# Kernel tuning notes

Measured on AMD Instinct MI355X. Metric: run time of the kernel, lower is better.

Reference implementation:

```python
import jax, jax.numpy as jnp
import numpy as np

B, T, INPUT, HIDDEN = 512, 128, 64, 512
TS, PLEN = 32, 32  # attention window (time_step), decode length (predict_len)


def setup_inputs() -> dict:
    key = jax.random.key(0)
    ks = jax.random.split(key, 11)
    s = 1.0 / np.sqrt(HIDDEN)
    rn = lambda k, shape, sc: (jax.random.normal(k, shape, jnp.float32) * sc)
    return {
        "x": jax.random.normal(ks[0], (B, T, INPUT), jnp.float32),
        "W_ih": rn(ks[1], (4 * HIDDEN, INPUT), s),
        "W_hh": rn(ks[2], (4 * HIDDEN, HIDDEN), s),
        "b_lstm": rn(ks[3], (4 * HIDDEN,), s),   # b_ih + b_hh folded together
        "Wc_ih": rn(ks[4], (4 * HIDDEN, HIDDEN), s),
        "Wc_hh": rn(ks[5], (4 * HIDDEN, HIDDEN), s),
        "b_cell": rn(ks[6], (4 * HIDDEN,), s),
        "W1": rn(ks[7], (HIDDEN, 2 * HIDDEN), s),
        "b1": rn(ks[8], (HIDDEN,), s),
        "W2": rn(ks[9], (1, HIDDEN), s),
        "b2": rn(ks[10], (1,), s),
    }


def _gates_to_hc(g, c):
    # torch gate order: input, forget, cell(g), output
    i, f, gg, o = jnp.split(g, 4, axis=-1)
    c_new = jax.nn.sigmoid(f) * c + jax.nn.sigmoid(i) * jnp.tanh(gg)
    h_new = jax.nn.sigmoid(o) * jnp.tanh(c_new)
    return h_new, c_new


def reference(x, W_ih, W_hh, b_lstm, Wc_ih, Wc_hh, b_cell, W1, b1, W2, b2):
    Bx = x.shape[0]
    # ---- encoder LSTM (single layer, zero init state) ----
    x_proj = jnp.einsum('bti,gi->btg', x, W_ih) + b_lstm  # [B,T,4H]

    def enc_step(carry, xt):
        h, c = carry
        h, c = _gates_to_hc(xt + h @ W_hh.T, c)
        return (h, c), h

    z = jnp.zeros((Bx, HIDDEN), x.dtype)
    (h, c), Hs = jax.lax.scan(enc_step, (z, z), x_proj.transpose(1, 0, 2))
    Hs = Hs.transpose(1, 0, 2)  # [B,T,H]

    # ---- decode loop: LSTMCell fed its own hidden + local windowed attention ----
    # Atten only ever reads the last TS states before the newest one, so we keep
    # a rolling buffer instead of materializing the growing H.
    Wc = Wc_ih + Wc_hh  # cell input == hidden state, so the two projections fuse
    buf0 = Hs[:, -TS:, :]  # last TS encoder states

    def dec_step(carry, _):
        h, c, buf = carry
        h_t, c_t = _gates_to_hc(h @ Wc.T + b_cell, c)
        scores = jnp.einsum('bh,bsh->bs', h_t, buf)        # [B,TS]
        a = jax.nn.softmax(scores, axis=-1)
        ctx = jnp.einsum('bs,bsh->bh', a, buf)             # [B,H]
        out = jnp.concatenate([ctx, h_t], axis=-1)         # [B,2H]
        buf = jnp.concatenate([buf[:, 1:], h_t[:, None]], axis=1)
        return (h_t, c_t, buf), out

    _, outs = jax.lax.scan(dec_step, (h, c, buf0), None, length=PLEN)
    H_pre = outs.transpose(1, 0, 2)  # [B,PLEN,2H]

    # ---- fc head (dropout = eval/identity) ----
    y = jnp.tanh(H_pre @ W1.T + b1) @ W2.T + b2  # [B,PLEN,1]
    return y.squeeze(-1)
```

## Files before the change

### kernel.cpp

```cpp
#include <hip/hip_runtime.h>
#include <hip/hip_bf16.h>
#include <math.h>

#define Bz   512
#define Tz   128
#define INz  64
#define Hz   512
#define TSz  32
#define PLz  32
#define BH   (Bz * Hz)
#define NBLK 256
#define NTHR 512
#define PF   6

typedef unsigned short u16;
typedef unsigned long long u64;
typedef __attribute__((ext_vector_type(8)))  short short8;
typedef __attribute__((ext_vector_type(16))) float floatx16;

static __device__ __forceinline__ void split_bf(float w, u16& hi, u16& lo) {
    __hip_bfloat16 h = __float2bfloat16(w);
    hi = *reinterpret_cast<u16*>(&h);
    float r = w - __bfloat162float(h);
    __hip_bfloat16 l = __float2bfloat16(r);
    lo = *reinterpret_cast<u16*>(&l);
}

union FU  { unsigned u; float f; };
union F2U { u64 q; float f[2]; };

static __device__ __forceinline__ float b2f(u16 v) {
    FU c; c.u = ((unsigned)v) << 16; return c.f;
}
static __device__ __forceinline__ u16 f2b(float f) {
    __hip_bfloat16 h = __float2bfloat16(f);
    return *reinterpret_cast<u16*>(&h);
}

static __device__ __forceinline__ float aldf(const float* p) {
    FU c; c.u = __hip_atomic_load((const unsigned*)p, __ATOMIC_RELAXED, __HIP_MEMORY_SCOPE_AGENT);
    return c.f;
}
static __device__ __forceinline__ void ast64f(float* p, float a, float b) {
    F2U u; u.f[0] = a; u.f[1] = b;
    __hip_atomic_store((u64*)p, u.q, __ATOMIC_RELAXED, __HIP_MEMORY_SCOPE_AGENT);
}
static __device__ __forceinline__ void astf(float* p, float v) {
    FU c; c.f = v;
    __hip_atomic_store((unsigned*)p, c.u, __ATOMIC_RELAXED, __HIP_MEMORY_SCOPE_AGENT);
}
static __device__ __forceinline__ unsigned aldu(const unsigned* p) {
    return __hip_atomic_load(p, __ATOMIC_RELAXED, __HIP_MEMORY_SCOPE_AGENT);
}
static __device__ __forceinline__ void astu(unsigned* p, unsigned v) {
    __hip_atomic_store(p, v, __ATOMIC_RELAXED, __HIP_MEMORY_SCOPE_AGENT);
}
static __device__ __forceinline__ void astu16x2(u16* p, unsigned v) {
    __hip_atomic_store((unsigned*)p, v, __ATOMIC_RELAXED, __HIP_MEMORY_SCOPE_AGENT);
}

__global__ __launch_bounds__(256) void k_init(u16* __restrict__ h15_hi,
                                              u16* __restrict__ h15_lo,
                                              unsigned* __restrict__ sync) {
    const int i = blockIdx.x * 256 + threadIdx.x;
    if (i < BH) { h15_hi[i] = 0; h15_lo[i] = 0; }
    if (i < 8192) sync[i] = 0;
}

__global__ __launch_bounds__(256) void k_prep_wenc(const float* __restrict__ W_ih,
                                                   const float* __restrict__ W_hh,
                                                   u16* __restrict__ wf_hi,
                                                   u16* __restrict__ wf_lo) {
    const int idx = blockIdx.x * 256 + threadIdx.x;
    const int lane = idx & 63;
    const int g = (idx >> 6) % 36;
    const int cb = idx / (36 * 64);
    const int C = cb * 32 + (lane & 31);
    const int gate = ((C >> 4) & 3) * 512 + (C >> 6) * 16 + (C & 15);
    const int kh = lane >> 5;
    const size_t base = (size_t)idx * 8;
    #pragma unroll
    for (int e = 0; e < 8; ++e) {
        const int k = g * 16 + kh * 8 + e;
        const float w = (k < 64) ? W_ih[(size_t)gate * 64 + k]
                                 : W_hh[(size_t)gate * 512 + (k - 64)];
        u16 hi, lo; split_bf(w, hi, lo);
        wf_hi[base + e] = hi; wf_lo[base + e] = lo;
    }
}

__global__ __launch_bounds__(256) void k_prep_wc(const float* __restrict__ Wc_ih,
                                                 const float* __restrict__ Wc_hh,
                                                 u16* __restrict__ wf_hi,
                                                 u16* __restrict__ wf_lo) {
    const int idx = blockIdx.x * 256 + threadIdx.x;
    const int lane = idx & 63;
    const int cb = idx / (32 * 64);
    const int g = (idx >> 6) % 32;
    const int C = cb * 32 + (lane & 31);
    const int gate = ((C >> 4) & 3) * 512 + (C >> 6) * 16 + (C & 15);
    const int kh = lane >> 5;
    const size_t base = (size_t)idx * 8;
    #pragma unroll
    for (int e = 0; e < 8; ++e) {
        const int k = g * 16 + kh * 8 + e;
        const float w = Wc_ih[(size_t)gate * 512 + k] + Wc_hh[(size_t)gate * 512 + k];
        u16 hi, lo; split_bf(w, hi, lo);
        wf_hi[base + e] = hi; wf_lo[base + e] = lo;
    }
}

__global__ __launch_bounds__(256) void k_prep_w1(const float* __restrict__ W1,
                                                 u16* __restrict__ wf_hi,
                                                 u16* __restrict__ wf_lo) {
    const int idx = blockIdx.x * 256 + threadIdx.x;
    const int lane = idx & 63;
    const int cb = idx / (64 * 64);
    const int g = (idx >> 6) % 64;
    const int n = cb * 32 + (lane & 31);
    const int kh = lane >> 5;
    const size_t base = (size_t)idx * 8;
    #pragma unroll
    for (int e = 0; e < 8; ++e) {
        const int k = g * 16 + kh * 8 + e;
        const float w = W1[(size_t)n * 1024 + k];
        u16 hi, lo; split_bf(w, hi, lo);
        wf_hi[base + e] = hi; wf_lo[base + e] = lo;
    }
}

__global__ __launch_bounds__(256) void k_prep_x(const float* __restrict__ x,
                                                u16* __restrict__ xf_hi,
                                                u16* __restrict__ xf_lo) {
    const int idx = blockIdx.x * 256 + threadIdx.x;
    const int lane = idx & 63;
    const int g = (idx >> 6) & 3;
    const int rb = (idx >> 8) & 15;
    const int t = idx >> 12;
    const int b = rb * 32 + (lane & 31);
    const int kh = lane >> 5;
    const size_t base = (size_t)idx * 8;
    #pragma unroll
    for (int e = 0; e < 8; ++e) {
        const int i = g * 16 + kh * 8 + e;
        const float w = x[((size_t)b * Tz + t) * INz + i];
        u16 hi, lo; split_bf(w, hi, lo);
        xf_hi[base + e] = hi; xf_lo[base + e] = lo;
    }
}

static __device__ __forceinline__ void gsync(unsigned* sync, unsigned target, int bid) {
    __syncthreads();
    const int tid = threadIdx.x;
    unsigned* arr  = sync + 64;
    unsigned* grel = sync + 64 + 4096;
    if (bid == 0) {
        if (tid < 64) {
            if (tid == 0) astu(&arr[0], target);
            bool done = false;
            while (!done) {
                unsigned mn = 0xffffffffu;
                #pragma unroll
                for (int k = 0; k < 4; ++k) {
                    const unsigned v = aldu(&arr[(tid * 4 + k) * 16]);
                    mn = v < mn ? v : mn;
                }
                done = (bool)__all((int)(mn >= target));
                if (!done) __builtin_amdgcn_s_sleep(1);
            }
            if (tid < 16) astu(&grel[tid * 16], target);
        }
    } else {
        if (tid == 0) {
            astu(&arr[bid * 16], target);
            while (aldu(&grel[(bid >> 4) * 16]) < target)
                __builtin_amdgcn_s_sleep(1);
        }
    }
    if ((target & 15u) == 0u && tid == 0)
        __builtin_amdgcn_fence(__ATOMIC_ACQUIRE, "agent");
    __syncthreads();
}

template<int NG, int GX>
__device__ __forceinline__ void gates_phase(
    const u16* __restrict__ xf_hi, const u16* __restrict__ xf_lo, int t,
    const u16* __restrict__ wf_hi, const u16* __restrict__ wf_lo,
    const u16* __restrict__ hin_hi, const u16* __restrict__ hin_lo,
    const float* __restrict__ bias,
    float (&c2)[2], float* __restrict__ h_f32,
    u16* __restrict__ hout_hi, u16* __restrict__ hout_lo,
    u16* __restrict__ buf_enc, int slot,
    u16* A_hi, u16* A_lo, float* Gt, int ji, int bi, int tid)
{
    const int lane = tid & 63, wid = tid >> 6;
    const int wc = wid & 3, kh = wid >> 2;

    {
        float4 vh[4], vl[4];
        #pragma unroll
        for (int it = 0; it < 4; ++it) {
            const int sl = it * 512 + tid;
            const size_t off = ((size_t)bi * 32 + (sl >> 6)) * 512 + (size_t)(sl & 63) * 8;
            vh[it] = *(const float4*)(hin_hi + off);
            vl[it] = *(const float4*)(hin_lo + off);
        }
        #pragma unroll
        for (int it = 0; it < 4; ++it) {
            const int sl = it * 512 + tid;
            *(float4*)(A_hi + (size_t)sl * 8) = vh[it];
            *(float4*)(A_lo + (size_t)sl * 8) = vl[it];
        }
    }
    __syncthreads();

    constexpr int NGH = NG / 2;
    const int g0 = kh * NGH;
    const int cb = ji * 4 + wc;
    const u16* pbh = wf_hi + ((size_t)cb * NG) * 512 + lane * 8;
    const u16* pbl = wf_lo + ((size_t)cb * NG) * 512 + lane * 8;

    floatx16 acc0, acc1, acc2;
    #pragma unroll
    for (int i = 0; i < 16; ++i) { acc0[i] = 0.f; acc1[i] = 0.f; acc2[i] = 0.f; }

    short8 ah[PF], al[PF], bh[PF], bl[PF];

    #pragma unroll
    for (int i = 0; i < NGH + PF; ++i) {
        if (i >= PF) {
            const int s = (i - PF) % PF;
            acc0 = __builtin_amdgcn_mfma_f32_32x32x16_bf16(ah[s], bh[s], acc0, 0, 0, 0);
            acc1 = __builtin_amdgcn_mfma_f32_32x32x16_bf16(ah[s], bl[s], acc1, 0, 0, 0);
            acc2 = __builtin_amdgcn_mfma_f32_32x32x16_bf16(al[s], bh[s], acc2, 0, 0, 0);
        }
        if (i < NGH) {
            const int s = i % PF;
            const int g = g0 + i;
            if (GX > 0 && g < GX) {
                const size_t off = (((size_t)t * 16 + bi) * GX + g) * 512 + (size_t)lane * 8;
                ah[s] = *(const short8*)(xf_hi + off);
                al[s] = *(const short8*)(xf_lo + off);
            } else {
                const int gh = g - GX;
                ah[s] = *(const short8*)(A_hi + ((size_t)gh * 64 + lane) * 8);
                al[s] = *(const short8*)(A_lo + ((size_t)gh * 64 + lane) * 8);
            }
            bh[s] = *(const short8*)(pbh + (size_t)g * 512);
            bl[s] = *(const short8*)(pbl + (size_t)g * 512);
        }
    }
    #pragma unroll
    for (int i = 0; i < 16; ++i) acc0[i] += acc1[i] + acc2[i];

    __syncthreads();
    {
        const int col = wc * 32 + (lane & 31);
        const int rb4 = 4 * (lane >> 5);
        float* G = Gt + (size_t)kh * 4224;
        #pragma unroll
        for (int r = 0; r < 16; ++r)
            G[(rb4 + (r & 3) + 8 * (r >> 2)) * 132 + col] = acc0[r];
    }
    __syncthreads();

    {
        const int bl2 = tid >> 4, jq = tid & 15;
        const int b = bi * 32 + bl2;
        const int j0 = ji * 32 + jq * 2;
        float hn2[2];
        unsigned phi = 0, plo = 0;
        #pragma unroll
        for (int e = 0; e < 2; ++e) {
            const int jl = jq * 2 + e;
            const int Cl = ((jl >> 4) << 6) | (jl & 15);
            const float* gp = Gt + (size_t)bl2 * 132 + Cl;
            const float* gq = gp + 4224;
            const float gi = gp[0]  + gq[0]  + bias[j0 + e];
            const float gf = gp[16] + gq[16] + bias[512 + j0 + e];
            const float gg = gp[32] + gq[32] + bias[1024 + j0 + e];
            const float go = gp[48] + gq[48] + bias[1536 + j0 + e];
            const float si = 1.f / (1.f + __expf(-gi));
            const float sf = 1.f / (1.f + __expf(-gf));
            const float so = 1.f / (1.f + __expf(-go));
            const float cn = sf * c2[e] + si * tanhf(gg);
            const float hn = so * tanhf(cn);
            c2[e] = cn; hn2[e] = hn;
            u16 hi, lo; split_bf(hn, hi, lo);
            phi |= (unsigned)hi << (16 * e);
            plo |= (unsigned)lo << (16 * e);
        }
        const int gran = j0 >> 4;
        const int fl = ((j0 >> 3) & 1) * 32 + (b & 31);
        const size_t fo = (((size_t)bi * 32 + gran) * 64 + fl) * 8 + (j0 & 7);
        astu16x2(hout_hi + fo, phi);
        astu16x2(hout_lo + fo, plo);
        if (slot >= 0)
            astu16x2(buf_enc + ((size_t)b * TSz + slot) * Hz + j0, phi);
        if (h_f32 != nullptr)
            ast64f(h_f32 + (size_t)b * Hz + j0, hn2[0], hn2[1]);
    }
}

__device__ __forceinline__ void attn_phase(const float* __restrict__ h_f32,
                                           const u16* __restrict__ buf_enc,
                                           u16* __restrict__ buf_dec,
                                           u16* __restrict__ ctx_hi, u16* __restrict__ ctx_lo,
                                           int sd, float* lds, int bid, int tid) {
    const int grp = tid >> 8;
    const int t8 = tid & 255;
    const int b = bid * 2 + grp;
    float* sh = lds + grp * 544;
    float* sa = sh + 512;
    {
        const int i0 = t8 * 2;
        const float2 hv = *(const float2*)(h_f32 + (size_t)b * Hz + i0);
        sh[i0] = hv.x; sh[i0 + 1] = hv.y;
    }
    __syncthreads();
    {
        const int w = t8 >> 3, l8 = t8 & 7;
        const u16* v = (w < TSz - sd)
            ? buf_enc + ((size_t)b * TSz + (sd + w)) * Hz
            : buf_dec + (size_t)(w - TSz + sd) * BH + (size_t)b * Hz;
        float p = 0.f;
        #pragma unroll 4
        for (int k = 0; k < 16; ++k) {
            const int j = l8 * 4 + k * 32;
            const ushort4 q = *(const ushort4*)(v + j);
            p = fmaf(sh[j],     b2f(q.x), p);
            p = fmaf(sh[j + 1], b2f(q.y), p);
            p = fmaf(sh[j + 2], b2f(q.z), p);
            p = fmaf(sh[j + 3], b2f(q.w), p);
        }
        p += __shfl_xor(p, 1); p += __shfl_xor(p, 2); p += __shfl_xor(p, 4);
        if (l8 == 0) sa[w] = p;
    }
    __syncthreads();
    if (t8 < TSz) {
        const float v = sa[t8];
        float m = v;
        #pragma unroll
        for (int d = 1; d < 32; d <<= 1) m = fmaxf(m, __shfl_xor(m, d));
        const float e = __expf(v - m);
        float ss = e;
        #pragma unroll
        for (int d = 1; d < 32; d <<= 1) ss += __shfl_xor(ss, d);
        sa[t8] = e / ss;
    }
    __syncthreads();
    {
        const int j0 = t8 * 2;
        float a0 = 0.f, a1 = 0.f;
        for (int w2 = 0; w2 < TSz; ++w2) {
            const u16* vp = (w2 < TSz - sd)
                ? buf_enc + ((size_t)b * TSz + (sd + w2)) * Hz + j0
                : buf_dec + (size_t)(w2 - TSz + sd) * BH + (size_t)b * Hz + j0;
            const ushort2 vv = *(const ushort2*)vp;
            a0 = fmaf(sa[w2], b2f(vv.x), a0);
            a1 = fmaf(sa[w2], b2f(vv.y), a1);
        }
        u16 h0, l0, h1, l1;
        split_bf(a0, h0, l0); split_bf(a1, h1, l1);
        const int rb = b >> 5, gran = j0 >> 4;
        const int fl = ((j0 >> 3) & 1) * 32 + (b & 31);
        const size_t fo = (((size_t)rb * 32 + gran) * 64 + fl) * 8 + (j0 & 7);
        astu16x2(ctx_hi + fo, (unsigned)h0 | ((unsigned)h1 << 16));
        astu16x2(ctx_lo + fo, (unsigned)l0 | ((unsigned)l1 << 16));
    }
    {
        const int i0 = t8 * 2;
        const unsigned pk = (unsigned)f2b(sh[i0]) | ((unsigned)f2b(sh[i0 + 1]) << 16);
        astu16x2(buf_dec + (size_t)sd * BH + (size_t)b * Hz + i0, pk);
    }
}

__device__ __forceinline__ void mlp_phase(
    const u16* __restrict__ ctx_hi, const u16* __restrict__ ctx_lo,
    const u16* __restrict__ h_hi,   const u16* __restrict__ h_lo,
    const u16* __restrict__ w1_hi,  const u16* __restrict__ w1_lo,
    const float* __restrict__ b1, const float* __restrict__ W2,
    float* __restrict__ part_p, float* lds, int bid, int tid)
{
    const int lane = tid & 63, w = tid >> 6;
    const int ni = bid & 15, bi2 = bid >> 4;

    floatx16 acc0, acc1, acc2;
    #pragma unroll
    for (int i = 0; i < 16; ++i) { acc0[i] = 0.f; acc1[i] = 0.f; acc2[i] = 0.f; }

    short8 ah[4], al[4], bh[4], bl[4];

    #pragma unroll
    for (int i = 0; i < 8 + 4; ++i) {
        if (i >= 4) {
            const int s = (i - 4) & 3;
            acc0 = __builtin_amdgcn_mfma_f32_32x32x16_bf16(ah[s], bh[s], acc0, 0, 0, 0);
            acc1 = __builtin_amdgcn_mfma_f32_32x32x16_bf16(ah[s], bl[s], acc1, 0, 0, 0);
            acc2 = __builtin_amdgcn_mfma_f32_32x32x16_bf16(al[s], bh[s], acc2, 0, 0, 0);
        }
        if (i < 8) {
            const int s = i & 3;
            const int g = w * 8 + i;
            if (g < 32) {
                const size_t off = (((size_t)bi2 * 32 + g) * 64 + lane) * 8;
                ah[s] = *(const short8*)(ctx_hi + off);
                al[s] = *(const short8*)(ctx_lo + off);
            } else {
                const size_t off = (((size_t)bi2 * 32 + (g - 32)) * 64 + lane) * 8;
                ah[s] = *(const short8*)(h_hi + off);
                al[s] = *(const short8*)(h_lo + off);
            }
            const size_t boff = (((size_t)ni * 64 + g) * 64 + lane) * 8;
            bh[s] = *(const short8*)(w1_hi + boff);
            bl[s] = *(const short8*)(w1_lo + boff);
        }
    }
    #pragma unroll
    for (int i = 0; i < 16; ++i) acc0[i] += acc1[i] + acc2[i];

    {
        const int col = lane & 31;
        const int rb4 = 4 * (lane >> 5);
        #pragma unroll
        for (int r = 0; r < 16; ++r)
            lds[w * 1024 + (rb4 + (r & 3) + 8 * (r >> 2)) * 32 + col] = acc0[r];
    }
    __syncthreads();

    const int row = tid >> 4, l16 = tid & 15;
    float a = 0.f;
    #pragma unroll
    for (int jj = 0; jj < 2; ++jj) {
        const int col = l16 * 2 + jj;
        const int ncol = ni * 32 + col;
        float pre = b1[ncol];
        #pragma unroll
        for (int ww = 0; ww < 8; ++ww) pre += lds[ww * 1024 + row * 32 + col];
        a = fmaf(tanhf(pre), W2[ncol], a);
    }
    a += __shfl_xor(a, 1); a += __shfl_xor(a, 2);
    a += __shfl_xor(a, 4); a += __shfl_xor(a, 8);
    if (l16 == 0) astf(&part_p[ni * 512 + bi2 * 32 + row], a);
}

__device__ __forceinline__ void y_reduce(const float* __restrict__ part_p,
                                         const float* __restrict__ b2,
                                         float* __restrict__ y, int s, int bid, int tid) {
    if (tid < 2) {
        const int b = bid * 2 + tid;
        float a = b2[0];
        #pragma unroll
        for (int ni = 0; ni < 16; ++ni) a += aldf(&part_p[ni * 512 + b]);
        astf(&y[(size_t)b * PLz + s], a);
    }
}

struct KParams {
    const u16 *xf_hi, *xf_lo, *wf_hi, *wf_lo, *wcf_hi, *wcf_lo, *w1f_hi, *w1f_lo;
    const float *b_l, *b_c, *b1, *W2, *b2;
    float *h_f32rot, *part_p, *y;
    u16 *buf_enc, *buf_dec;
    u16 *hrot_hi, *hrot_lo, *ctxrot_hi, *ctxrot_lo;
    unsigned *sync;
};

__global__ __launch_bounds__(NTHR, 1) void k_persist(KParams p) {
    __shared__ char smem[65536];
    u16* A_hi = (u16*)smem;
    u16* A_lo = (u16*)(smem + 32768);
    float* Gt = (float*)smem;
    float* scr = (float*)smem;

    const int bid = blockIdx.x;
    const int tid = threadIdx.x;
    const int xcd = bid & 7, idx = bid >> 3;
    const int g_ji = (xcd & 1) | ((idx & 7) << 1);
    const int g_bi = ((xcd >> 1) & 3) | ((idx >> 3) << 2);
    unsigned gen = 1;
    float c2[2] = {0.f, 0.f};

    for (int t = 0; t < Tz; ++t) {
        const int si = (t + 15) & 15, so = t & 15;
        gates_phase<36, 4>(p.xf_hi, p.xf_lo, t, p.wf_hi, p.wf_lo,
                           p.hrot_hi + (size_t)si * BH, p.hrot_lo + (size_t)si * BH,
                           p.b_l, c2, nullptr,
                           p.hrot_hi + (size_t)so * BH, p.hrot_lo + (size_t)so * BH,
                           p.buf_enc, t - 96, A_hi, A_lo, Gt, g_ji, g_bi, tid);
        gsync(p.sync, gen++, bid);
    }
    for (int sd = 0; sd < PLz; ++sd) {
        if (sd > 0) y_reduce(p.part_p, p.b2, p.y, sd - 1, bid, tid);
        const int si = (sd + 15) & 15, so = sd & 15;
        float* hf = p.h_f32rot + (size_t)(sd & 7) * BH;
        u16* cx_hi = p.ctxrot_hi + (size_t)(sd & 7) * BH;
        u16* cx_lo = p.ctxrot_lo + (size_t)(sd & 7) * BH;
        gates_phase<32, 0>(nullptr, nullptr, 0, p.wcf_hi, p.wcf_lo,
                           p.hrot_hi + (size_t)si * BH, p.hrot_lo + (size_t)si * BH,
                           p.b_c, c2, hf,
                           p.hrot_hi + (size_t)so * BH, p.hrot_lo + (size_t)so * BH,
                           nullptr, -1, A_hi, A_lo, Gt, g_ji, g_bi, tid);
        gsync(p.sync, gen++, bid);
        attn_phase(hf, p.buf_enc, p.buf_dec, cx_hi, cx_lo, sd, scr, bid, tid);
        gsync(p.sync, gen++, bid);
        mlp_phase(cx_hi, cx_lo,
                  p.hrot_hi + (size_t)so * BH, p.hrot_lo + (size_t)so * BH,
                  p.w1f_hi, p.w1f_lo, p.b1, p.W2, p.part_p, scr, bid, tid);
        gsync(p.sync, gen++, bid);
    }
    y_reduce(p.part_p, p.b2, p.y, PLz - 1, bid, tid);
}

extern "C" void kernel_launch(void* const* d_in, const int* in_sizes, int n_in,
                              void* d_out, int out_size, void* d_ws, size_t ws_size,
                              hipStream_t stream) {
    (void)in_sizes; (void)n_in; (void)out_size; (void)ws_size;
    const float* x     = (const float*)d_in[0];
    const float* W_ih  = (const float*)d_in[1];
    const float* W_hh  = (const float*)d_in[2];
    const float* b_l   = (const float*)d_in[3];
    const float* Wc_ih = (const float*)d_in[4];
    const float* Wc_hh = (const float*)d_in[5];
    const float* b_c   = (const float*)d_in[6];
    const float* W1    = (const float*)d_in[7];
    const float* b1    = (const float*)d_in[8];
    const float* W2    = (const float*)d_in[9];
    const float* b2    = (const float*)d_in[10];
    float* y = (float*)d_out;

    float* w = (float*)d_ws;
    float* h_f32rot = w;
    float* part_p   = w + 8 * (size_t)BH;
    unsigned* sync  = (unsigned*)(w + 8 * (size_t)BH + 8192);
    u16* us = (u16*)(w + 8 * (size_t)BH + 8192 + 8192);
    u16* buf_enc = us;   us += 32 * (size_t)BH;
    u16* buf_dec = us;   us += 32 * (size_t)BH;
    u16* hrot_hi = us;   us += 16 * (size_t)BH;
    u16* hrot_lo = us;   us += 16 * (size_t)BH;
    u16* ctxrot_hi = us; us += 8 * (size_t)BH;
    u16* ctxrot_lo = us; us += 8 * (size_t)BH;
    u16* xf_hi = us;   us += 4194304;
    u16* xf_lo = us;   us += 4194304;
    u16* wf_hi = us;   us += 1179648;
    u16* wf_lo = us;   us += 1179648;
    u16* wcf_hi = us;  us += 1048576;
    u16* wcf_lo = us;  us += 1048576;
    u16* w1f_hi = us;  us += 524288;
    u16* w1f_lo = us;  us += 524288;

    k_init     <<<1024, 256, 0, stream>>>(hrot_hi + 15 * (size_t)BH,
                                          hrot_lo + 15 * (size_t)BH, sync);
    k_prep_wenc<<<576,  256, 0, stream>>>(W_ih, W_hh, wf_hi, wf_lo);
    k_prep_wc  <<<512,  256, 0, stream>>>(Wc_ih, Wc_hh, wcf_hi, wcf_lo);
    k_prep_w1  <<<256,  256, 0, stream>>>(W1, w1f_hi, w1f_lo);
    k_prep_x   <<<2048, 256, 0, stream>>>(x, xf_hi, xf_lo);

    KParams prm;
    prm.xf_hi = xf_hi;   prm.xf_lo = xf_lo;
    prm.wf_hi = wf_hi;   prm.wf_lo = wf_lo;
    prm.wcf_hi = wcf_hi; prm.wcf_lo = wcf_lo;
    prm.w1f_hi = w1f_hi; prm.w1f_lo = w1f_lo;
    prm.b_l = b_l; prm.b_c = b_c; prm.b1 = b1; prm.W2 = W2; prm.b2 = b2;
    prm.h_f32rot = h_f32rot; prm.part_p = part_p; prm.y = y;
    prm.buf_enc = buf_enc; prm.buf_dec = buf_dec;
    prm.hrot_hi = hrot_hi; prm.hrot_lo = hrot_lo;
    prm.ctxrot_hi = ctxrot_hi; prm.ctxrot_lo = ctxrot_lo;
    prm.sync = sync;

    k_persist<<<dim3(NBLK), dim3(NTHR), 0, stream>>>(prm);
}
```

Measured before the change: 2.169 ms.

## Replace master-gathered grid barrier with two-level atomic counter tree

The grid barrier used to have block 0 poll per-block arrival slots and release group flags. It now uses a two-level fetch-add tree: 16 group counters, then a root counter whose last arriver publishes the target to a single flag that every block spins on. This takes the serial gather-and-release through one block off the critical path of each step, at the cost of atomic contention and all blocks polling one cache line. Memory ordering still relies on relaxed atomics plus a periodic acquire fence, so visibility remains as delicate as before.

```diff
diff --git a/kernel.cpp b/kernel.cpp
--- a/kernel.cpp
+++ b/kernel.cpp
@@ -151,34 +151,20 @@
 
 static __device__ __forceinline__ void gsync(unsigned* sync, unsigned target, int bid) {
     __syncthreads();
-    const int tid = threadIdx.x;
-    unsigned* arr  = sync + 64;
-    unsigned* grel = sync + 64 + 4096;
-    if (bid == 0) {
-        if (tid < 64) {
-            if (tid == 0) astu(&arr[0], target);
-            bool done = false;
-            while (!done) {
-                unsigned mn = 0xffffffffu;
-                #pragma unroll
-                for (int k = 0; k < 4; ++k) {
-                    const unsigned v = aldu(&arr[(tid * 4 + k) * 16]);
-                    mn = v < mn ? v : mn;
-                }
-                done = (bool)__all((int)(mn >= target));
-                if (!done) __builtin_amdgcn_s_sleep(1);
-            }
-            if (tid < 16) astu(&grel[tid * 16], target);
-        }
-    } else {
-        if (tid == 0) {
-            astu(&arr[bid * 16], target);
-            while (aldu(&grel[(bid >> 4) * 16]) < target)
-                __builtin_amdgcn_s_sleep(1);
-        }
-    }
-    if ((target & 15u) == 0u && tid == 0)
-        __builtin_amdgcn_fence(__ATOMIC_ACQUIRE, "agent");
+    if (threadIdx.x == 0) {
+        unsigned* grp  = sync + 64 + ((bid >> 4) << 4);
+        unsigned* root = sync + 64 + (16 << 4);
+        const unsigned a = __hip_atomic_fetch_add(grp, 1u, __ATOMIC_RELAXED, __HIP_MEMORY_SCOPE_AGENT);
+        if ((a & 15u) == 15u) {
+            const unsigned r = __hip_atomic_fetch_add(root, 1u, __ATOMIC_RELAXED, __HIP_MEMORY_SCOPE_AGENT);
+            if ((r & 15u) == 15u)
+                astu(sync, target);
+        }
+        while (aldu(sync) < target)
+            __builtin_amdgcn_s_sleep(2);
+        if ((target & 15u) == 0u)
+            __builtin_amdgcn_fence(__ATOMIC_ACQUIRE, "agent");
+    }
     __syncthreads();
 }
 
```

After: 2.123 ms. 2.1% less time.
